# Kernel tuning notes

Hardware: AMD Instinct MI355X
Metric: run time of the kernel (lower is better)

Reference implementation:

```python
import jax, jax.numpy as jnp
from jax import lax
import numpy as np

RANK = 4
C_IN = 32
C_OUT = 64
H, W = 128, 256
L1 = (H + 2, W + 2)      # conv k=3, pad=2, stride=1 -> H+2
L2 = (L1[0] + 2, L1[1] + 2)
EPS = 1e-5


def setup_inputs() -> dict:
    key = jax.random.key(0)
    ks = jax.random.split(key, 12)
    s = lambda k, shp: jax.random.normal(k, shp, dtype=jnp.float32) * 0.05
    inp = {
        "x": jax.random.normal(ks[0], (16, C_IN, H, W), dtype=jnp.float32),
        # layer 1: rank basis kernels, bias, outer combining-weight logits
        "w1": s(ks[1], (RANK, C_OUT, C_IN, 3, 3)),
        "b1": jnp.zeros((C_OUT,), jnp.float32),
        "a1h": s(ks[2], (RANK, L1[0])),
        "a1w": s(ks[3], (RANK, L1[1])),
        "g1": jnp.ones((C_OUT,), jnp.float32),
        "be1": jnp.zeros((C_OUT,), jnp.float32),
        # layer 2
        "w2": s(ks[4], (RANK, C_OUT, C_OUT, 3, 3)),
        "b2": jnp.zeros((C_OUT,), jnp.float32),
        "a2h": s(ks[5], (RANK, L2[0])),
        "a2w": s(ks[6], (RANK, L2[1])),
        "g2": jnp.ones((C_OUT,), jnp.float32),
        "be2": jnp.zeros((C_OUT,), jnp.float32),
    }
    return inp


def _combining_weights(ah, aw):
    # outer sum of row/col logits, softmax over rank -> [rank, Lh, Lw]
    return jax.nn.softmax(ah[:, :, None] + aw[:, None, :], axis=0)


def _lrlc(x, w, b, cw):
    # x: [B, Cin, H, W]; w: [rank, Cout, Cin, 3, 3]; cw: [rank, H', W']
    rank, co, ci, kh, kw = w.shape
    y = lax.conv_general_dilated(
        x, w.reshape(rank * co, ci, kh, kw),
        window_strides=(1, 1), padding=[(2, 2), (2, 2)],
        dimension_numbers=("NCHW", "OIHW", "NCHW"))
    B, _, Ho, Wo = y.shape
    y = y.reshape(B, rank, co, Ho, Wo)
    return jnp.einsum("brohw,rhw->bohw", y, cw) + b[None, :, None, None]


def _bn_relu(x, g, be):
    # training-mode BatchNorm2d (batch stats, biased variance) + ReLU
    mean = jnp.mean(x, axis=(0, 2, 3), keepdims=True)
    var = jnp.var(x, axis=(0, 2, 3), keepdims=True)
    xn = (x - mean) * lax.rsqrt(var + EPS)
    return jax.nn.relu(xn * g[None, :, None, None] + be[None, :, None, None])


def _maxpool3(x):
    return lax.reduce_window(x, -jnp.inf, lax.max,
                             (1, 1, 3, 3), (1, 1, 3, 3), "VALID")


def reference(x, w1, b1, a1h, a1w, g1, be1, w2, b2, a2h, a2w, g2, be2):
    cw1 = _combining_weights(a1h, a1w)
    h = _lrlc(x, w1, b1, cw1)
    h = _bn_relu(h, g1, be1)
    cw2 = _combining_weights(a2h, a2w)
    h = _lrlc(h, w2, b2, cw2)
    h = _bn_relu(h, g2, be2)
    return _maxpool3(h)
```

## Files before the change

### kernel.cpp

```cpp
#include <hip/hip_runtime.h>
#include <hip/hip_bf16.h>
#include <math.h>

#define COUT 64
#define EPS  1e-5f

typedef __hip_bfloat16 bf16;
typedef short  short8  __attribute__((ext_vector_type(8)));
typedef short  short4v __attribute__((ext_vector_type(4)));
typedef float  floatx4 __attribute__((ext_vector_type(4)));

__device__ __forceinline__ short bf16_bits(float f) {
    union { __hip_bfloat16 h; short s; } u;
    u.h = __float2bfloat16(f);
    return u.s;
}
__device__ __forceinline__ float bits_to_f32(short s) {
    union { __hip_bfloat16 h; short s; } u;
    u.s = s;
    return __bfloat162float(u.h);
}

#define NV1   33800
#define NV2   34584
#define XPAD_PLANE  (132*260)
#define H1_PLANE    (134*262)
#define H2_PLANE    (132*260)
#define NPOS1 (16*130*258)
#define NPOS2 (16*132*260)

__global__ void zero_f_kernel(float* __restrict__ p, int n) {
    int i = blockIdx.x*blockDim.x + threadIdx.x;
    if (i < n) p[i] = 0.f;
}
__global__ void zero4_kernel(uint4* __restrict__ p, long n4) {
    long i = (long)blockIdx.x*blockDim.x + threadIdx.x;
    for (; i < n4; i += (long)gridDim.x*blockDim.x) p[i] = make_uint4(0,0,0,0);
}

__global__ void cwv_kernel(const float* __restrict__ ah, const float* __restrict__ aw,
                           float* __restrict__ cwv, int Nv, int Wv, int Lh, int Lw) {
    int idx = blockIdx.x*blockDim.x + threadIdx.x;
    if (idx >= Nv) return;
    int oh = idx / Wv, ow = idx - oh*Wv;
    if (ow > Lw-1) ow = Lw-1;
    float v0 = ah[0*Lh+oh] + aw[0*Lw+ow];
    float v1 = ah[1*Lh+oh] + aw[1*Lw+ow];
    float v2 = ah[2*Lh+oh] + aw[2*Lw+ow];
    float v3 = ah[3*Lh+oh] + aw[3*Lw+ow];
    float m = fmaxf(fmaxf(v0,v1), fmaxf(v2,v3));
    v0 = __expf(v0-m); v1 = __expf(v1-m); v2 = __expf(v2-m); v3 = __expf(v3-m);
    float inv = 1.f/(v0+v1+v2+v3);
    cwv[0*(size_t)Nv+idx] = v0*inv; cwv[1*(size_t)Nv+idx] = v1*inv;
    cwv[2*(size_t)Nv+idx] = v2*inv; cwv[3*(size_t)Nv+idx] = v3*inv;
}

template<int CIN_, int NSLICES>
__global__ void pack_kernel(const float* __restrict__ w, short* __restrict__ Apk) {
    int gid = blockIdx.x*256 + threadIdx.x;
    if (gid >= NSLICES*1024) return;
    int l = gid & 63, t = (gid >> 6) & 15, s = gid >> 10;
    int m = t*16 + (l & 15);
    int r = m >> 6, co = m & 63;
    int kbase = s*32 + ((l >> 4) << 3);
    short8 v;
    #pragma unroll
    for (int j = 0; j < 8; ++j) {
        int k = kbase + j;
        int tap = k / CIN_, ci = k % CIN_;
        v[j] = bf16_bits(w[(((size_t)(r*COUT + co))*CIN_ + ci)*9 + tap]);
    }
    *reinterpret_cast<short8*>(Apk + (size_t)gid*8) = v;
}

__global__ void xpad_kernel(const float* __restrict__ x, short* __restrict__ xp) {
    int row = blockIdx.x;
    int b = row / 132, ih = row - b*132;
    int ci = threadIdx.x & 31, iw0 = threadIdx.x >> 5;
    for (int iw = iw0; iw < 260; iw += 8) {
        float v = 0.f;
        if (ih >= 2 && ih < 130 && iw >= 2 && iw < 258)
            v = x[(((size_t)b*32 + ci)*128 + (ih-2))*256 + (iw-2)];
        xp[((size_t)row*260 + iw)*32 + ci] = bf16_bits(v);
    }
}

template<int CIN_, int NSLICES>
__launch_bounds__(256, 2)
__global__ void lrlc_conv(const short* __restrict__ Bpl, const short* __restrict__ Apk,
                          const float* __restrict__ cwv, const float* __restrict__ bias,
                          short* __restrict__ Out, float* __restrict__ sum, float* __restrict__ sq,
                          int Wv, int Hout, int Wreal, int Nv, int inPlanePos,
                          int outW, int outPlanePos, int outPad) {
    const int tid  = threadIdx.x;
    const int w    = tid >> 6, l = tid & 63;
    const int quad = l >> 4, l15 = l & 15;
    const int b    = blockIdx.y;
    const int n0   = blockIdx.x * 128;

    __shared__ float cwS[4*128];
    for (int t = tid; t < 512; t += 256) {
        int r = t >> 7, nn = t & 127;
        int n = n0 + nn; if (n > Nv-1) n = Nv-1;
        cwS[t] = cwv[(size_t)r*Nv + n];
    }
    __syncthreads();

    const short* Bb = Bpl + (size_t)b*inPlanePos*CIN_;
    int bOff[8];
    #pragma unroll
    for (int j = 0; j < 8; ++j) bOff[j] = (n0 + j*16 + l15)*CIN_ + quad*8;
    const short* Aw = Apk + (size_t)(w*64 + l)*8;

    floatx4 acc[4][8];
    #pragma unroll
    for (int i = 0; i < 4; ++i)
        #pragma unroll
        for (int j = 0; j < 8; ++j)
            acc[i][j] = (floatx4){0.f,0.f,0.f,0.f};

    #pragma unroll
    for (int s = 0; s < NSLICES; ++s) {
        const int tap = (CIN_ == 32) ? s : (s >> 1);
        const int cb  = (CIN_ == 32) ? 0 : ((s & 1) << 5);
        const int koff = ((tap/3)*Wv + (tap%3))*CIN_ + cb;
        short8 bfr[8], afr[4];
        #pragma unroll
        for (int j = 0; j < 8; ++j)
            bfr[j] = *reinterpret_cast<const short8*>(Bb + bOff[j] + koff);
        #pragma unroll
        for (int i = 0; i < 4; ++i)
            afr[i] = *reinterpret_cast<const short8*>(Aw + (size_t)(s*16 + i*4)*512);
        #pragma unroll
        for (int i = 0; i < 4; ++i)
            #pragma unroll
            for (int j = 0; j < 8; ++j)
                acc[i][j] = __builtin_amdgcn_mfma_f32_16x16x32_bf16(afr[i], bfr[j], acc[i][j], 0, 0, 0);
    }

    const int co_base = w*16 + quad*4;
    float bs[4];
    #pragma unroll
    for (int rg = 0; rg < 4; ++rg) bs[rg] = bias[co_base + rg];
    float st[4] = {0.f,0.f,0.f,0.f}, st2[4] = {0.f,0.f,0.f,0.f};
    #pragma unroll
    for (int j = 0; j < 8; ++j) {
        int nl = j*16 + l15;
        int n  = n0 + nl;
        int oh = n / Wv, ow = n - oh*Wv;
        bool valid = (ow < Wreal) && (oh < Hout);
        float c0 = cwS[nl], c1 = cwS[128+nl], c2 = cwS[256+nl], c3 = cwS[384+nl];
        short4v pk;
        #pragma unroll
        for (int rg = 0; rg < 4; ++rg) {
            float v = acc[0][j][rg]*c0 + acc[1][j][rg]*c1
                    + acc[2][j][rg]*c2 + acc[3][j][rg]*c3 + bs[rg];
            if (valid) { st[rg] += v; st2[rg] = fmaf(v, v, st2[rg]); }
            pk[rg] = bf16_bits(v);
        }
        if (valid) {
            size_t op = ((size_t)b*outPlanePos + (size_t)(oh + outPad)*outW + (ow + outPad))*(size_t)COUT + co_base;
            *reinterpret_cast<short4v*>(Out + op) = pk;
        }
    }
    #pragma unroll
    for (int m = 1; m < 16; m <<= 1) {
        #pragma unroll
        for (int rg = 0; rg < 4; ++rg) {
            st[rg]  += __shfl_xor(st[rg],  m, 16);
            st2[rg] += __shfl_xor(st2[rg], m, 16);
        }
    }
    if (l15 == 0) {
        #pragma unroll
        for (int rg = 0; rg < 4; ++rg) {
            atomicAdd(&sum[co_base+rg], st[rg]);
            atomicAdd(&sq[co_base+rg],  st2[rg]);
        }
    }
}

__global__ void finalize_kernel(const float* __restrict__ sum, const float* __restrict__ sumsq,
                                const float* __restrict__ g, const float* __restrict__ be,
                                float* __restrict__ A, float* __restrict__ Bc, float cnt) {
    int c = threadIdx.x;
    if (c >= COUT) return;
    float mean = sum[c]/cnt;
    float var  = sumsq[c]/cnt - mean*mean;
    float inv  = rsqrtf(var + EPS);
    float a = g[c]*inv;
    A[c]  = a;
    Bc[c] = fmaf(-mean, a, be[c]);
}

__global__ void bnrelu_rows(short* __restrict__ h, const float* __restrict__ A,
                            const float* __restrict__ Bc) {
    __shared__ float sA[64], sB[64];
    if (threadIdx.x < 64) { sA[threadIdx.x] = A[threadIdx.x]; sB[threadIdx.x] = Bc[threadIdx.x]; }
    __syncthreads();
    int row = blockIdx.x;
    int b = row / 130, oh = row - b*130;
    short* base = h + ((size_t)(b*134 + oh + 2)*262 + 2)*64;
    const int nvec = 258*64/8;
    for (int it = threadIdx.x; it < nvec; it += 256) {
        short8 d = *reinterpret_cast<short8*>(base + it*8);
        int c0 = (it*8) & 63;
        #pragma unroll
        for (int q = 0; q < 8; ++q) {
            float v = bits_to_f32(d[q]);
            int c = c0 + q;
            v = fmaxf(fmaf(v, sA[c], sB[c]), 0.f);
            d[q] = bf16_bits(v);
        }
        *reinterpret_cast<short8*>(base + it*8) = d;
    }
}

__global__ void maxpool_rows(const short* __restrict__ h2, const float* __restrict__ A,
                             const float* __restrict__ Bc, float* __restrict__ out) {
    __shared__ float sA[64], sB[64];
    if (threadIdx.x < 64) { sA[threadIdx.x] = A[threadIdx.x]; sB[threadIdx.x] = Bc[threadIdx.x]; }
    __syncthreads();
    int row = blockIdx.x;
    int b = row / 44, ph = row - b*44;
    for (int item = threadIdx.x; item < 86*16; item += 256) {
        int cg = item & 15, pw = item >> 4;
        float m[4] = {0.f,0.f,0.f,0.f};
        #pragma unroll
        for (int i = 0; i < 3; ++i) {
            const short* rp = h2 + ((size_t)(b*132 + ph*3 + i)*260 + pw*3)*64 + cg*4;
            #pragma unroll
            for (int j = 0; j < 3; ++j) {
                short4v d = *reinterpret_cast<const short4v*>(rp + j*64);
                #pragma unroll
                for (int q = 0; q < 4; ++q) {
                    int c = cg*4 + q;
                    float v = fmaf(bits_to_f32(d[q]), sA[c], sB[c]);
                    m[q] = fmaxf(m[q], v);
                }
            }
        }
        #pragma unroll
        for (int q = 0; q < 4; ++q)
            out[((size_t)(b*64 + cg*4 + q)*44 + ph)*86 + pw] = m[q];
    }
}

extern "C" void kernel_launch(void* const* d_in, const int* in_sizes, int n_in,
                              void* d_out, int out_size, void* d_ws, size_t ws_size,
                              hipStream_t stream) {
    const float* x   = (const float*)d_in[0];
    const float* w1  = (const float*)d_in[1];
    const float* b1  = (const float*)d_in[2];
    const float* a1h = (const float*)d_in[3];
    const float* a1w = (const float*)d_in[4];
    const float* g1  = (const float*)d_in[5];
    const float* be1 = (const float*)d_in[6];
    const float* w2  = (const float*)d_in[7];
    const float* b2  = (const float*)d_in[8];
    const float* a2h = (const float*)d_in[9];
    const float* a2w = (const float*)d_in[10];
    const float* g2  = (const float*)d_in[11];
    const float* be2 = (const float*)d_in[12];
    float* out = (float*)d_out;

    char* ws = (char*)d_ws;
    float* stats = (float*)ws;
    float* sum1 = stats;       float* sq1 = stats + 64;
    float* A1   = stats + 128; float* Bc1 = stats + 192;
    float* sum2 = stats + 256; float* sq2 = stats + 320;
    float* A2   = stats + 384; float* Bc2 = stats + 448;
    float* cw1v = (float*)(ws + 2048);
    float* cw2v = cw1v + 4*NV1;
    short* Apk1 = (short*)(cw2v + 4*NV2);
    short* Apk2 = Apk1 + 73728;
    short* h1pad = Apk2 + 147456;
    short* xpad  = h1pad + (size_t)16*H1_PLANE*64 + 4096;
    short* h2    = xpad;

    zero_f_kernel<<<2, 256, 0, stream>>>(stats, 512);
    {
        long n4 = ((size_t)16*H1_PLANE*64 + 4096) * 2 / 16;
        zero4_kernel<<<4096, 256, 0, stream>>>((uint4*)h1pad, n4);
    }
    cwv_kernel<<<(NV1+255)/256, 256, 0, stream>>>(a1h, a1w, cw1v, NV1, 260, 130, 258);
    cwv_kernel<<<(NV2+255)/256, 256, 0, stream>>>(a2h, a2w, cw2v, NV2, 262, 132, 260);
    pack_kernel<32, 9><<<(9*1024+255)/256, 256, 0, stream>>>(w1, Apk1);
    pack_kernel<64,18><<<(18*1024+255)/256, 256, 0, stream>>>(w2, Apk2);
    xpad_kernel<<<16*132, 256, 0, stream>>>(x, xpad);

    lrlc_conv<32, 9><<<dim3((NV1+127)/128, 16), 256, 0, stream>>>(
        xpad, Apk1, cw1v, b1, h1pad, sum1, sq1,
        260, 130, 258, NV1, XPAD_PLANE, 262, H1_PLANE, 2);
    finalize_kernel<<<1, 64, 0, stream>>>(sum1, sq1, g1, be1, A1, Bc1, (float)NPOS1);
    bnrelu_rows<<<16*130, 256, 0, stream>>>(h1pad, A1, Bc1);

    lrlc_conv<64,18><<<dim3((NV2+127)/128, 16), 256, 0, stream>>>(
        h1pad, Apk2, cw2v, b2, h2, sum2, sq2,
        262, 132, 260, NV2, H1_PLANE, 260, H2_PLANE, 0);
    finalize_kernel<<<1, 64, 0, stream>>>(sum2, sq2, g2, be2, A2, Bc2, (float)NPOS2);

    maxpool_rows<<<16*44, 256, 0, stream>>>(h2, A2, Bc2, out);
}
```

Before: 1.186 ms.

## Tile conv input into LDS with 2D output blocks and fuse prep kernels

```diff
diff --git a/kernel.cpp b/kernel.cpp
--- a/kernel.cpp
+++ b/kernel.cpp
@@ -21,43 +21,36 @@
     return __bfloat162float(u.h);
 }
 
-#define NV1   33800
-#define NV2   34584
-#define XPAD_PLANE  (132*260)
 #define H1_PLANE    (134*262)
 #define H2_PLANE    (132*260)
 #define NPOS1 (16*130*258)
 #define NPOS2 (16*132*260)
-
-__global__ void zero_f_kernel(float* __restrict__ p, int n) {
-    int i = blockIdx.x*blockDim.x + threadIdx.x;
-    if (i < n) p[i] = 0.f;
-}
-__global__ void zero4_kernel(uint4* __restrict__ p, long n4) {
-    long i = (long)blockIdx.x*blockDim.x + threadIdx.x;
-    for (; i < n4; i += (long)gridDim.x*blockDim.x) p[i] = make_uint4(0,0,0,0);
-}
-
-__global__ void cwv_kernel(const float* __restrict__ ah, const float* __restrict__ aw,
-                           float* __restrict__ cwv, int Nv, int Wv, int Lh, int Lw) {
-    int idx = blockIdx.x*blockDim.x + threadIdx.x;
-    if (idx >= Nv) return;
-    int oh = idx / Wv, ow = idx - oh*Wv;
-    if (ow > Lw-1) ow = Lw-1;
-    float v0 = ah[0*Lh+oh] + aw[0*Lw+ow];
-    float v1 = ah[1*Lh+oh] + aw[1*Lw+ow];
-    float v2 = ah[2*Lh+oh] + aw[2*Lw+ow];
-    float v3 = ah[3*Lh+oh] + aw[3*Lw+ow];
+#define CW1_N (130*258)
+#define CW2_N (132*260)
+
+#define CW1_BLK ((CW1_N + 255)/256)
+#define CW2_BLK ((CW2_N + 255)/256)
+#define PK1_BLK (9*1024/256)
+#define PK2_BLK (18*1024/256)
+
+__device__ __forceinline__ void cw_body(const float* __restrict__ ah, const float* __restrict__ aw,
+                                        float* __restrict__ cw, int Lh, int Lw, int idx) {
+    int n = Lh*Lw;
+    if (idx >= n) return;
+    int i = idx / Lw, j = idx - i*Lw;
+    float v0 = ah[0*Lh+i] + aw[0*Lw+j];
+    float v1 = ah[1*Lh+i] + aw[1*Lw+j];
+    float v2 = ah[2*Lh+i] + aw[2*Lw+j];
+    float v3 = ah[3*Lh+i] + aw[3*Lw+j];
     float m = fmaxf(fmaxf(v0,v1), fmaxf(v2,v3));
     v0 = __expf(v0-m); v1 = __expf(v1-m); v2 = __expf(v2-m); v3 = __expf(v3-m);
     float inv = 1.f/(v0+v1+v2+v3);
-    cwv[0*(size_t)Nv+idx] = v0*inv; cwv[1*(size_t)Nv+idx] = v1*inv;
-    cwv[2*(size_t)Nv+idx] = v2*inv; cwv[3*(size_t)Nv+idx] = v3*inv;
+    cw[0*n+idx] = v0*inv; cw[1*n+idx] = v1*inv;
+    cw[2*n+idx] = v2*inv; cw[3*n+idx] = v3*inv;
 }
 
 template<int CIN_, int NSLICES>
-__global__ void pack_kernel(const float* __restrict__ w, short* __restrict__ Apk) {
-    int gid = blockIdx.x*256 + threadIdx.x;
+__device__ __forceinline__ void pack_body(const float* __restrict__ w, short* __restrict__ Apk, int gid) {
     if (gid >= NSLICES*1024) return;
     int l = gid & 63, t = (gid >> 6) & 15, s = gid >> 10;
     int m = t*16 + (l & 15);
@@ -73,44 +66,89 @@
     *reinterpret_cast<short8*>(Apk + (size_t)gid*8) = v;
 }
 
-__global__ void xpad_kernel(const float* __restrict__ x, short* __restrict__ xp) {
-    int row = blockIdx.x;
-    int b = row / 132, ih = row - b*132;
-    int ci = threadIdx.x & 31, iw0 = threadIdx.x >> 5;
-    for (int iw = iw0; iw < 260; iw += 8) {
-        float v = 0.f;
-        if (ih >= 2 && ih < 130 && iw >= 2 && iw < 258)
-            v = x[(((size_t)b*32 + ci)*128 + (ih-2))*256 + (iw-2)];
-        xp[((size_t)row*260 + iw)*32 + ci] = bf16_bits(v);
+__global__ void prep_kernel(const float* __restrict__ a1h, const float* __restrict__ a1w,
+                            const float* __restrict__ a2h, const float* __restrict__ a2w,
+                            const float* __restrict__ w1, const float* __restrict__ w2,
+                            float* __restrict__ stats, float* __restrict__ cw1,
+                            float* __restrict__ cw2, short* __restrict__ Apk1,
+                            short* __restrict__ Apk2) {
+    int bx = blockIdx.x;
+    if (bx == 0) {
+        stats[threadIdx.x] = 0.f; stats[threadIdx.x + 256] = 0.f;
+    } else if (bx < 1 + CW1_BLK) {
+        cw_body(a1h, a1w, cw1, 130, 258, (bx-1)*256 + threadIdx.x);
+    } else if (bx < 1 + CW1_BLK + CW2_BLK) {
+        cw_body(a2h, a2w, cw2, 132, 260, (bx-(1+CW1_BLK))*256 + threadIdx.x);
+    } else if (bx < 1 + CW1_BLK + CW2_BLK + PK1_BLK) {
+        pack_body<32, 9>(w1, Apk1, (bx-(1+CW1_BLK+CW2_BLK))*256 + threadIdx.x);
+    } else {
+        pack_body<64,18>(w2, Apk2, (bx-(1+CW1_BLK+CW2_BLK+PK1_BLK))*256 + threadIdx.x);
+    }
+}
+#define PREP_BLOCKS (1 + CW1_BLK + CW2_BLK + PK1_BLK + PK2_BLK)
+
+#define ZBLK 2048
+__global__ void zero_xpad_kernel(uint4* __restrict__ h1p, long n4,
+                                 const float* __restrict__ x, short* __restrict__ xp) {
+    if (blockIdx.x < ZBLK) {
+        for (long i = (long)blockIdx.x*256 + threadIdx.x; i < n4; i += (long)ZBLK*256)
+            h1p[i] = make_uint4(0,0,0,0);
+    } else {
+        int row = blockIdx.x - ZBLK;
+        int b = row / 132, ih = row - b*132;
+        int ci = threadIdx.x & 31, iw0 = threadIdx.x >> 5;
+        for (int iw = iw0; iw < 260; iw += 8) {
+            float v = 0.f;
+            if (ih >= 2 && ih < 130 && iw >= 2 && iw < 258)
+                v = x[(((size_t)b*32 + ci)*128 + (ih-2))*256 + (iw-2)];
+            xp[((size_t)row*260 + iw)*32 + ci] = bf16_bits(v);
+        }
     }
 }
 
 template<int CIN_, int NSLICES>
 __launch_bounds__(256, 2)
 __global__ void lrlc_conv(const short* __restrict__ Bpl, const short* __restrict__ Apk,
-                          const float* __restrict__ cwv, const float* __restrict__ bias,
+                          const float* __restrict__ cw, const float* __restrict__ bias,
                           short* __restrict__ Out, float* __restrict__ sum, float* __restrict__ sq,
-                          int Wv, int Hout, int Wreal, int Nv, int inPlanePos,
-                          int outW, int outPlanePos, int outPad) {
+                          int Hin, int Win, int Hout, int Wout,
+                          int outW, int outPlane, int outPad) {
+    constexpr int GSH = (CIN_ == 64) ? 3 : 2;
+    constexpr int GPC = 1 << GSH;
+    constexpr int TILE_SLOTS = 6*34*GPC;
+    __shared__ short tile[TILE_SLOTS*8];
+    __shared__ float cwS[512];
+
     const int tid  = threadIdx.x;
     const int w    = tid >> 6, l = tid & 63;
     const int quad = l >> 4, l15 = l & 15;
-    const int b    = blockIdx.y;
-    const int n0   = blockIdx.x * 128;
-
-    __shared__ float cwS[4*128];
+    const int b    = blockIdx.z;
+    const int ow0  = blockIdx.x * 32;
+    const int oh0  = blockIdx.y * 4;
+
     for (int t = tid; t < 512; t += 256) {
-        int r = t >> 7, nn = t & 127;
-        int n = n0 + nn; if (n > Nv-1) n = Nv-1;
-        cwS[t] = cwv[(size_t)r*Nv + n];
+        int r = t >> 7, n = t & 127;
+        int oh = min(oh0 + (n >> 5), Hout-1);
+        int ow = min(ow0 + (n & 31), Wout-1);
+        cwS[t] = cw[((size_t)r*Hout + oh)*Wout + ow];
+    }
+    const short* Bb = Bpl + (size_t)b*Hin*Win*CIN_;
+    for (int slot = tid; slot < TILE_SLOTS; slot += 256) {
+        int g  = slot & (GPC-1); int cu = slot >> GSH;
+        int rr = cu / 34, cc = cu - rr*34;
+        int ih = min(oh0 + rr, Hin-1);
+        int ic = min(ow0 + cc, Win-1);
+        *reinterpret_cast<short8*>(&tile[slot*8]) =
+            *reinterpret_cast<const short8*>(Bb + ((size_t)ih*Win + ic)*CIN_ + g*8);
     }
     __syncthreads();
 
-    const short* Bb = Bpl + (size_t)b*inPlanePos*CIN_;
-    int bOff[8];
-    #pragma unroll
-    for (int j = 0; j < 8; ++j) bOff[j] = (n0 + j*16 + l15)*CIN_ + quad*8;
-    const short* Aw = Apk + (size_t)(w*64 + l)*8;
+    int base0[8];
+    #pragma unroll
+    for (int j = 0; j < 8; ++j) {
+        int n = j*16 + l15;
+        base0[j] = (((n >> 5)*34 + (n & 31)) << GSH) + quad;
+    }
 
     floatx4 acc[4][8];
     #pragma unroll
@@ -122,15 +160,16 @@
     #pragma unroll
     for (int s = 0; s < NSLICES; ++s) {
         const int tap = (CIN_ == 32) ? s : (s >> 1);
-        const int cb  = (CIN_ == 32) ? 0 : ((s & 1) << 5);
-        const int koff = ((tap/3)*Wv + (tap%3))*CIN_ + cb;
-        short8 bfr[8], afr[4];
+        const int g0  = (CIN_ == 32) ? 0 : ((s & 1) << 2);
+        const int koff = (((tap/3)*34 + (tap%3)) << GSH) + g0;
+        short8 afr[4], bfr[8];
+        #pragma unroll
+        for (int i = 0; i < 4; ++i)
+            afr[i] = *reinterpret_cast<const short8*>(
+                Apk + (size_t)s*8192 + i*2048 + w*512 + l*8);
         #pragma unroll
         for (int j = 0; j < 8; ++j)
-            bfr[j] = *reinterpret_cast<const short8*>(Bb + bOff[j] + koff);
-        #pragma unroll
-        for (int i = 0; i < 4; ++i)
-            afr[i] = *reinterpret_cast<const short8*>(Aw + (size_t)(s*16 + i*4)*512);
+            bfr[j] = *reinterpret_cast<const short8*>(&tile[(base0[j] + koff)*8]);
         #pragma unroll
         for (int i = 0; i < 4; ++i)
             #pragma unroll
@@ -145,11 +184,10 @@
     float st[4] = {0.f,0.f,0.f,0.f}, st2[4] = {0.f,0.f,0.f,0.f};
     #pragma unroll
     for (int j = 0; j < 8; ++j) {
-        int nl = j*16 + l15;
-        int n  = n0 + nl;
-        int oh = n / Wv, ow = n - oh*Wv;
-        bool valid = (ow < Wreal) && (oh < Hout);
-        float c0 = cwS[nl], c1 = cwS[128+nl], c2 = cwS[256+nl], c3 = cwS[384+nl];
+        int n  = j*16 + l15;
+        int oh = oh0 + (n >> 5), ow = ow0 + (n & 31);
+        bool valid = (oh < Hout) && (ow < Wout);
+        float c0 = cwS[n], c1 = cwS[128+n], c2 = cwS[256+n], c3 = cwS[384+n];
         short4v pk;
         #pragma unroll
         for (int rg = 0; rg < 4; ++rg) {
@@ -159,7 +197,7 @@
             pk[rg] = bf16_bits(v);
         }
         if (valid) {
-            size_t op = ((size_t)b*outPlanePos + (size_t)(oh + outPad)*outW + (ow + outPad))*(size_t)COUT + co_base;
+            size_t op = ((size_t)b*outPlane + (size_t)(oh + outPad)*outW + (ow + outPad))*(size_t)COUT + co_base;
             *reinterpret_cast<short4v*>(Out + op) = pk;
         }
     }
@@ -270,34 +308,32 @@
     float* A1   = stats + 128; float* Bc1 = stats + 192;
     float* sum2 = stats + 256; float* sq2 = stats + 320;
     float* A2   = stats + 384; float* Bc2 = stats + 448;
-    float* cw1v = (float*)(ws + 2048);
-    float* cw2v = cw1v + 4*NV1;
-    short* Apk1 = (short*)(cw2v + 4*NV2);
+    float* cw1 = (float*)(ws + 2048);
+    float* cw2 = cw1 + 4*CW1_N;
+    short* Apk1 = (short*)(cw2 + 4*CW2_N);
     short* Apk2 = Apk1 + 73728;
     short* h1pad = Apk2 + 147456;
     short* xpad  = h1pad + (size_t)16*H1_PLANE*64 + 4096;
     short* h2    = xpad;
 
-    zero_f_kernel<<<2, 256, 0, stream>>>(stats, 512);
+    prep_kernel<<<PREP_BLOCKS, 256, 0, stream>>>(a1h, a1w, a2h, a2w, w1, w2,
+                                                 stats, cw1, cw2, Apk1, Apk2);
     {
-        long n4 = ((size_t)16*H1_PLANE*64 + 4096) * 2 / 16;
-        zero4_kernel<<<4096, 256, 0, stream>>>((uint4*)h1pad, n4);
-    }
-    cwv_kernel<<<(NV1+255)/256, 256, 0, stream>>>(a1h, a1w, cw1v, NV1, 260, 130, 258);
-    cwv_kernel<<<(NV2+255)/256, 256, 0, stream>>>(a2h, a2w, cw2v, NV2, 262, 132, 260);
-    pack_kernel<32, 9><<<(9*1024+255)/256, 256, 0, stream>>>(w1, Apk1);
-    pack_kernel<64,18><<<(18*1024+255)/256, 256, 0, stream>>>(w2, Apk2);
-    xpad_kernel<<<16*132, 256, 0, stream>>>(x, xpad);
-
-    lrlc_conv<32, 9><<<dim3((NV1+127)/128, 16), 256, 0, stream>>>(
-        xpad, Apk1, cw1v, b1, h1pad, sum1, sq1,
-        260, 130, 258, NV1, XPAD_PLANE, 262, H1_PLANE, 2);
+        long n4 = ((size_t)16*H1_PLANE*64) * 2 / 16;
+        zero_xpad_kernel<<<ZBLK + 16*132, 256, 0, stream>>>((uint4*)h1pad, n4, x, xpad);
+    }
+
+    lrlc_conv<32, 9><<<dim3(9, 33, 16), 256, 0, stream>>>(
+        xpad, Apk1, cw1, b1, h1pad, sum1, sq1,
+        132, 260, 130, 258,
+        262, H1_PLANE, 2);
     finalize_kernel<<<1, 64, 0, stream>>>(sum1, sq1, g1, be1, A1, Bc1, (float)NPOS1);
     bnrelu_rows<<<16*130, 256, 0, stream>>>(h1pad, A1, Bc1);
 
-    lrlc_conv<64,18><<<dim3((NV2+127)/128, 16), 256, 0, stream>>>(
-        h1pad, Apk2, cw2v, b2, h2, sum2, sq2,
-        262, 132, 260, NV2, H1_PLANE, 260, H2_PLANE, 0);
+    lrlc_conv<64,18><<<dim3(9, 33, 16), 256, 0, stream>>>(
+        h1pad, Apk2, cw2, b2, h2, sum2, sq2,
+        134, 262, 132, 260,
+        260, H2_PLANE, 0);
     finalize_kernel<<<1, 64, 0, stream>>>(sum2, sq2, g2, be2, A2, Bc2, (float)NPOS2);
 
     maxpool_rows<<<16*44, 256, 0, stream>>>(h2, A2, Bc2, out);
```

New measurement: 1.226 ms. 3.4% more time.
